# Kernel tuning notes

Measured on AMD Instinct MI355X. Metric: run time of the kernel, lower is better.

## Reference

```python
import jax, jax.numpy as jnp
import numpy as np

T, B, F_, H, D, C = 16, 1024, 512, 128, 8, 100  # trees, batch, feat, hidden, depth, classes
L = 2 ** (D + 1)  # n_leaf = 512


def _routing_tables():
    # Static per-leaf routing: node index and branch side at each depth.
    # Derived from compute_mu's gather indices:
    #   node(d, l) = 2^d - 1 + l // 2^(D+1-d);  side(d, l) = (l // 2^(D-d)) % 2
    l = np.arange(L)
    node = np.stack([(2 ** d - 1) + l // (2 ** (D + 1 - d)) for d in range(D + 1)])  # [D+1, L]
    side = np.stack([(l // (2 ** (D - d))) % 2 for d in range(D + 1)])               # [D+1, L]
    return jnp.asarray(node, dtype=jnp.int32), jnp.asarray(side.astype(np.bool_))


def setup_inputs() -> dict:
    key = jax.random.key(0)
    ks = jax.random.split(key, 4)
    return {
        "feat": jax.random.normal(ks[0], (B, F_), jnp.float32),
        "W1": jax.random.normal(ks[1], (T, F_, H), jnp.float32) * 0.05,
        "b1": jnp.zeros((T, H), jnp.float32),
        "W2": jax.random.normal(ks[2], (T, H, L), jnp.float32) * 0.05,
        "b2": jnp.zeros((T, L), jnp.float32),
        "pi": jax.random.uniform(ks[3], (T, L, C), jnp.float32, -2.0, 2.0),
    }


def reference(feat, W1, b1, W2, b2, pi):
    node, side = _routing_tables()
    # Per-tree MLP head (dropout is identity in eval mode).
    h = jax.nn.relu(jnp.einsum('bf,tfh->tbh', feat, W1) + b1[:, None, :])        # [T,B,H]
    p = jax.nn.sigmoid(jnp.einsum('tbh,thl->tbl', h, W2) + b2[:, None, :])       # [T,B,L]
    # compute_mu: product of routing probs along each root->leaf path.
    sel = p[:, :, node]                          # [T,B,D+1,L] gather (static indices)
    route = jnp.where(side, 1.0 - sel, sel)      # left -> p, right -> 1-p
    mu = jnp.prod(route, axis=2)                 # [T,B,L]
    # compute_py_x: mean over leaves then mean over trees of mu @ softmax(pi).
    leaf_p = jax.nn.softmax(pi, axis=-1)         # [T,L,C]
    py_x = jnp.einsum('tbl,tlc->bc', mu, leaf_p) / (L * T)  # [B,C]
    return jnp.log(py_x)
```

## Files before the change

### kernel.cpp

```cpp
#include <hip/hip_runtime.h>
#include <hip/hip_bf16.h>
#include <math.h>

#define T_ 16
#define B_ 1024
#define F_ 512
#define H_ 128
#define D_ 8
#define C_ 100
#define L_ 512
#define CP_ 112

typedef __attribute__((ext_vector_type(8))) short bf16x8_t;
typedef __attribute__((ext_vector_type(4))) short bf16x4_t;
typedef __attribute__((ext_vector_type(4))) float f32x4_t;

__device__ inline ushort f2bf(float x) {
  __hip_bfloat16 b = __float2bfloat16(x);
  return *(ushort*)&b;
}
__device__ inline float bf2f(ushort u) {
  union { unsigned int i; float f; } v;
  v.i = ((unsigned int)u) << 16;
  return v.f;
}

__global__ __launch_bounds__(256) void k_prep(
    const float* __restrict__ feat, const float* __restrict__ W1,
    const float* __restrict__ W2, const float* __restrict__ pi,
    ushort* __restrict__ feat_bf, ushort* __restrict__ W1T,
    ushort* __restrict__ W2T, ushort* __restrict__ lp) {
  __shared__ float tile[32][33];
  const int bid = blockIdx.x, tid = threadIdx.x;

  if (bid < 256) {
    int i = (bid * 256 + tid) * 8;
    float4 a = *(const float4*)(feat + i);
    float4 b = *(const float4*)(feat + i + 4);
    bf16x8_t o;
    o[0] = (short)f2bf(a.x); o[1] = (short)f2bf(a.y);
    o[2] = (short)f2bf(a.z); o[3] = (short)f2bf(a.w);
    o[4] = (short)f2bf(b.x); o[5] = (short)f2bf(b.y);
    o[6] = (short)f2bf(b.z); o[7] = (short)f2bf(b.w);
    *(bf16x8_t*)(feat_bf + i) = o;
    return;
  }
  if (bid < 2304) {
    const float* X; ushort* XT; int K, N, kb, nb, s;
    if (bid < 1280) {
      int r = bid - 256;  kb = r & 15; nb = (r >> 4) & 3;  s = r >> 6;
      X = W1; XT = W1T; K = F_; N = H_;
    } else {
      int r = bid - 1280; kb = r & 3;  nb = (r >> 2) & 15; s = r >> 6;
      X = W2; XT = W2T; K = H_; N = L_;
    }
    const int k0 = kb * 32, n0 = nb * 32;
    const int c = tid & 31, r0 = tid >> 5;
    const float* Xs = X + (size_t)s * K * N;
    ushort* XTs = XT + (size_t)s * N * K;
#pragma unroll
    for (int j = 0; j < 4; ++j)
      tile[r0 + 8 * j][c] = Xs[(size_t)(k0 + r0 + 8 * j) * N + n0 + c];
    __syncthreads();
#pragma unroll
    for (int j = 0; j < 4; ++j)
      XTs[(size_t)(n0 + r0 + 8 * j) * K + k0 + c] = f2bf(tile[c][r0 + 8 * j]);
    return;
  }
  {
    int row  = (bid - 2304) * 4 + (tid >> 6);
    int lane = tid & 63;
    const float* x = pi + (size_t)row * C_;
    float v0 = (lane < C_) ? x[lane] : -1e30f;
    float v1 = (lane + 64 < C_) ? x[lane + 64] : -1e30f;
    float m = fmaxf(v0, v1);
#pragma unroll
    for (int off = 32; off; off >>= 1) m = fmaxf(m, __shfl_xor(m, off, 64));
    float e0 = __expf(v0 - m);
    float e1 = (lane + 64 < C_) ? __expf(v1 - m) : 0.0f;
    float sm = e0 + e1;
#pragma unroll
    for (int off = 32; off; off >>= 1) sm += __shfl_xor(sm, off, 64);
    float inv = 1.0f / sm;
    size_t base = (size_t)row * CP_;
    if (lane < C_) lp[base + lane] = f2bf(e0 * inv);
    int c2 = lane + 64;
    if (c2 < CP_) lp[base + c2] = f2bf(c2 < C_ ? e1 * inv : 0.0f);
  }
}

__global__ __launch_bounds__(256) void k12_mfma(
    const ushort* __restrict__ feat, const ushort* __restrict__ W1T,
    const float* __restrict__ b1, const ushort* __restrict__ W2T,
    const float* __restrict__ b2, ushort* __restrict__ mu) {
  __shared__ ushort smem[29696];
  ushort (*h_s)[136] = (ushort(*)[136])smem;
  ushort (*a_s)[72]  = (ushort(*)[72])(smem + 4352);
  ushort (*b_s)[72]  = (ushort(*)[72])(smem + 6656);
  ushort (*w_s)[136] = (ushort(*)[136])(smem + 4352);
  ushort (*p_s)[520] = (ushort(*)[520])(smem + 13056);

  const int t = blockIdx.y, b0 = blockIdx.x * 32, tid = threadIdx.x;
  const int w = tid >> 6, lane = tid & 63, quad = lane >> 4, n = lane & 15;

  {
    f32x4_t acc[2][2];
#pragma unroll
    for (int i = 0; i < 2; ++i)
#pragma unroll
      for (int j = 0; j < 2; ++j) acc[i][j] = (f32x4_t){0.f, 0.f, 0.f, 0.f};

    for (int kc = 0; kc < 8; ++kc) {
      __syncthreads();
      {
        int row = tid >> 3, col8 = (tid & 7) * 8;
        *(bf16x8_t*)&a_s[row][col8] =
            *(const bf16x8_t*)(feat + (size_t)(b0 + row) * F_ + kc * 64 + col8);
      }
#pragma unroll
      for (int i = 0; i < 4; ++i) {
        int idx = i * 256 + tid;
        int row = idx >> 3, col8 = (idx & 7) * 8;
        *(bf16x8_t*)&b_s[row][col8] =
            *(const bf16x8_t*)(W1T + ((size_t)t * H_ + row) * F_ + kc * 64 + col8);
      }
      __syncthreads();
#pragma unroll
      for (int ks = 0; ks < 64; ks += 32) {
        bf16x8_t af[2], bfr[2];
#pragma unroll
        for (int mt = 0; mt < 2; ++mt)
          af[mt] = *(const bf16x8_t*)&a_s[mt * 16 + n][ks + quad * 8];
#pragma unroll
        for (int nt = 0; nt < 2; ++nt)
          bfr[nt] = *(const bf16x8_t*)&b_s[w * 32 + nt * 16 + n][ks + quad * 8];
#pragma unroll
        for (int mt = 0; mt < 2; ++mt)
#pragma unroll
          for (int nt = 0; nt < 2; ++nt)
            acc[mt][nt] = __builtin_amdgcn_mfma_f32_16x16x32_bf16(
                af[mt], bfr[nt], acc[mt][nt], 0, 0, 0);
      }
    }
    float bias[2] = {b1[t * H_ + w * 32 + n], b1[t * H_ + w * 32 + 16 + n]};
#pragma unroll
    for (int mt = 0; mt < 2; ++mt)
#pragma unroll
      for (int nt = 0; nt < 2; ++nt)
#pragma unroll
        for (int r = 0; r < 4; ++r) {
          int row = mt * 16 + quad * 4 + r;
          int col = w * 32 + nt * 16 + n;
          float v = acc[mt][nt][r] + bias[nt];
          h_s[row][col] = f2bf(v > 0.f ? v : 0.f);
        }
  }

  for (int nc = 0; nc < 8; ++nc) {
    __syncthreads();
#pragma unroll
    for (int i = 0; i < 4; ++i) {
      int idx = i * 256 + tid;
      int row = idx >> 4, col8 = (idx & 15) * 8;
      *(bf16x8_t*)&w_s[row][col8] =
          *(const bf16x8_t*)(W2T + ((size_t)t * L_ + nc * 64 + row) * H_ + col8);
    }
    __syncthreads();
    f32x4_t acc[2];
    acc[0] = (f32x4_t){0.f, 0.f, 0.f, 0.f};
    acc[1] = (f32x4_t){0.f, 0.f, 0.f, 0.f};
#pragma unroll
    for (int ks = 0; ks < 128; ks += 32) {
      bf16x8_t bfrag = *(const bf16x8_t*)&w_s[w * 16 + n][ks + quad * 8];
#pragma unroll
      for (int mt = 0; mt < 2; ++mt) {
        bf16x8_t afrag = *(const bf16x8_t*)&h_s[mt * 16 + n][ks + quad * 8];
        acc[mt] = __builtin_amdgcn_mfma_f32_16x16x32_bf16(afrag, bfrag,
                                                          acc[mt], 0, 0, 0);
      }
    }
    int l = nc * 64 + w * 16 + n;
    float bias = b2[t * L_ + l];
#pragma unroll
    for (int mt = 0; mt < 2; ++mt)
#pragma unroll
      for (int r = 0; r < 4; ++r) {
        float x = acc[mt][r] + bias;
        p_s[mt * 16 + quad * 4 + r][l] = f2bf(1.0f / (1.0f + __expf(-x)));
      }
  }
  __syncthreads();

#pragma unroll
  for (int pass = 0; pass < 4; ++pass) {
    int b = pass * 8 + (tid >> 5);
    int s = tid & 31;
    float P = 1.f;
#pragma unroll
    for (int d = 0; d < 5; ++d) {
      int nd = (1 << d) - 1 + (s >> (5 - d));
      int sd = (s >> (4 - d)) & 1;
      float pv = bf2f(p_s[b][nd]);
      P *= sd ? (1.f - pv) : pv;
    }
    float p5 = bf2f(p_s[b][31 + s]);
    float q5[2] = {P * p5, P * (1.f - p5)};
    float q6[4], q7[8];
#pragma unroll
    for (int j = 0; j < 2; ++j) {
      float pv = bf2f(p_s[b][63 + 2 * s + j]);
      q6[2 * j] = q5[j] * pv;
      q6[2 * j + 1] = q5[j] * (1.f - pv);
    }
#pragma unroll
    for (int u = 0; u < 4; ++u) {
      float pv = bf2f(p_s[b][127 + 4 * s + u]);
      q7[2 * u] = q6[u] * pv;
      q7[2 * u + 1] = q6[u] * (1.f - pv);
    }
    bf16x8_t o0, o1;
#pragma unroll
    for (int v = 0; v < 8; ++v) {
      float pv = bf2f(p_s[b][255 + 8 * s + v]);
      ushort e0 = f2bf(q7[v] * pv);
      ushort e1 = f2bf(q7[v] * (1.f - pv));
      if (v < 4) { o0[2 * v] = (short)e0; o0[2 * v + 1] = (short)e1; }
      else       { o1[2 * (v - 4)] = (short)e0; o1[2 * (v - 4) + 1] = (short)e1; }
    }
    ushort* dst = mu + ((size_t)t * B_ + b0 + b) * L_ + s * 16;
    *(bf16x8_t*)dst = o0;
    *(bf16x8_t*)(dst + 8) = o1;
  }
}

__global__ __launch_bounds__(256) void k5_mfma(
    const ushort* __restrict__ mu, const ushort* __restrict__ lp,
    float* __restrict__ part) {
  __shared__ ushort bT[CP_ * 68];
  const int t   = blockIdx.y;
  const int m0  = blockIdx.x * 64;
  const int tid = threadIdx.x;
  const int wave = tid >> 6, lane = tid & 63;
  const int quad = lane >> 4;
  const int n    = lane & 15;
  const int mrow = m0 + wave * 16 + n;

  f32x4_t acc[7];
#pragma unroll
  for (int i = 0; i < 7; ++i) acc[i] = (f32x4_t){0.f, 0.f, 0.f, 0.f};

  const ushort* muRow = mu + ((size_t)t * B_ + mrow) * L_;
  const ushort* lp_t  = lp + (size_t)t * L_ * CP_;

  for (int k0 = 0; k0 < L_; k0 += 64) {
    __syncthreads();
#pragma unroll
    for (int i = 0; i < 28; ++i) {
      int e  = i * 256 + tid;
      int kk = e / CP_;
      int c  = e - kk * CP_;
      bT[c * 68 + kk] = lp_t[(size_t)(k0 + kk) * CP_ + c];
    }
    __syncthreads();
#pragma unroll
    for (int ks = 0; ks < 64; ks += 32) {
      bf16x8_t afrag = *(const bf16x8_t*)(muRow + k0 + ks + quad * 8);
#pragma unroll
      for (int nt = 0; nt < 7; ++nt) {
        const ushort* bb = &bT[(nt * 16 + n) * 68 + ks + quad * 8];
        bf16x4_t lo = *(const bf16x4_t*)(bb);
        bf16x4_t hi = *(const bf16x4_t*)(bb + 4);
        bf16x8_t bfrag;
#pragma unroll
        for (int j = 0; j < 4; ++j) { bfrag[j] = lo[j]; bfrag[4 + j] = hi[j]; }
        acc[nt] = __builtin_amdgcn_mfma_f32_16x16x32_bf16(afrag, bfrag, acc[nt], 0, 0, 0);
      }
    }
  }
#pragma unroll
  for (int nt = 0; nt < 7; ++nt) {
    int c = nt * 16 + n;
    if (c < C_) {
#pragma unroll
      for (int r = 0; r < 4; ++r) {
        int m = m0 + wave * 16 + quad * 4 + r;
        part[((size_t)t * B_ + m) * C_ + c] = acc[nt][r];
      }
    }
  }
}

__global__ __launch_bounds__(256) void k6_log(
    const float* __restrict__ part, float* __restrict__ out) {
  int i = blockIdx.x * 256 + threadIdx.x;
  if (i < B_ * C_) {
    float s = 0.0f;
#pragma unroll
    for (int t = 0; t < T_; ++t) s += part[(size_t)t * B_ * C_ + i];
    out[i] = logf(s * (1.0f / (L_ * T_)));
  }
}

extern "C" void kernel_launch(void* const* d_in, const int* in_sizes, int n_in,
                              void* d_out, int out_size, void* d_ws,
                              size_t ws_size, hipStream_t stream) {
  const float* feat = (const float*)d_in[0];
  const float* W1   = (const float*)d_in[1];
  const float* b1   = (const float*)d_in[2];
  const float* W2   = (const float*)d_in[3];
  const float* b2   = (const float*)d_in[4];
  const float* pi   = (const float*)d_in[5];
  float* out = (float*)d_out;

  char* ws = (char*)d_ws;
  ushort* feat_bf  = (ushort*)(ws);
  ushort* W1T_buf  = (ushort*)(ws + ((size_t)1 << 20));
  ushort* W2T_buf  = (ushort*)(ws + ((size_t)3 << 20));
  ushort* mu_buf   = (ushort*)(ws + ((size_t)5 << 20));
  ushort* leaf_buf = (ushort*)(ws + ((size_t)21 << 20));
  float*  part_buf = (float*)(ws + ((size_t)23 << 20));

  k_prep<<<4352, 256, 0, stream>>>(feat, W1, W2, pi, feat_bf, W1T_buf,
                                   W2T_buf, leaf_buf);
  k12_mfma<<<dim3(B_ / 32, T_), 256, 0, stream>>>(feat_bf, W1T_buf, b1,
                                                  W2T_buf, b2, mu_buf);
  k5_mfma<<<dim3(B_ / 64, T_), 256, 0, stream>>>(mu_buf, leaf_buf, part_buf);
  k6_log<<<(B_ * C_ + 255) / 256, 256, 0, stream>>>(part_buf, out);
}
```

Baseline: 114.5 us.

## Fuse leaf-probability GEMM into routing kernel, keep mu in shared memory

The mu @ softmax(pi) GEMM moves into the MLP/routing kernel. The mu tile is written to shared memory over the p_s buffer and consumed directly by MFMA, so the 16 MB bf16 mu array no longer goes to global memory and one kernel launch is removed. The leaf softmax is now stored transposed ([T, C, L]) so B fragments load straight from global memory with no LDS transpose. In exchange, every 32-row block re-reads the per-tree leaf matrix from global/L2, the wave split is uneven (4 vs 3 column tiles), and the prep kernel's transposed writes are strided.

```diff
diff --git a/kernel.cpp b/kernel.cpp
--- a/kernel.cpp
+++ b/kernel.cpp
@@ -29,7 +29,7 @@
     const float* __restrict__ feat, const float* __restrict__ W1,
     const float* __restrict__ W2, const float* __restrict__ pi,
     ushort* __restrict__ feat_bf, ushort* __restrict__ W1T,
-    ushort* __restrict__ W2T, ushort* __restrict__ lp) {
+    ushort* __restrict__ W2T, ushort* __restrict__ lpT) {
   __shared__ float tile[32][33];
   const int bid = blockIdx.x, tid = threadIdx.x;
 
@@ -70,6 +70,7 @@
   {
     int row  = (bid - 2304) * 4 + (tid >> 6);
     int lane = tid & 63;
+    int t = row >> 9, l = row & (L_ - 1);
     const float* x = pi + (size_t)row * C_;
     float v0 = (lane < C_) ? x[lane] : -1e30f;
     float v1 = (lane + 64 < C_) ? x[lane + 64] : -1e30f;
@@ -82,17 +83,18 @@
 #pragma unroll
     for (int off = 32; off; off >>= 1) sm += __shfl_xor(sm, off, 64);
     float inv = 1.0f / sm;
-    size_t base = (size_t)row * CP_;
-    if (lane < C_) lp[base + lane] = f2bf(e0 * inv);
+    ushort* dst = lpT + (size_t)t * CP_ * L_ + l;
+    if (lane < C_) dst[(size_t)lane * L_] = f2bf(e0 * inv);
     int c2 = lane + 64;
-    if (c2 < CP_) lp[base + c2] = f2bf(c2 < C_ ? e1 * inv : 0.0f);
+    if (c2 < CP_) dst[(size_t)c2 * L_] = f2bf(c2 < C_ ? e1 * inv : 0.0f);
   }
 }
 
 __global__ __launch_bounds__(256) void k12_mfma(
     const ushort* __restrict__ feat, const ushort* __restrict__ W1T,
     const float* __restrict__ b1, const ushort* __restrict__ W2T,
-    const float* __restrict__ b2, ushort* __restrict__ mu) {
+    const float* __restrict__ b2, const ushort* __restrict__ lpT,
+    float* __restrict__ part) {
   __shared__ ushort smem[29696];
   ushort (*h_s)[136] = (ushort(*)[136])smem;
   ushort (*a_s)[72]  = (ushort(*)[72])(smem + 4352);
@@ -191,6 +193,7 @@
   }
   __syncthreads();
 
+  bf16x8_t mo[4][2];
 #pragma unroll
   for (int pass = 0; pass < 4; ++pass) {
     int b = pass * 8 + (tid >> 5);
@@ -227,64 +230,49 @@
       if (v < 4) { o0[2 * v] = (short)e0; o0[2 * v + 1] = (short)e1; }
       else       { o1[2 * (v - 4)] = (short)e0; o1[2 * (v - 4) + 1] = (short)e1; }
     }
-    ushort* dst = mu + ((size_t)t * B_ + b0 + b) * L_ + s * 16;
-    *(bf16x8_t*)dst = o0;
-    *(bf16x8_t*)(dst + 8) = o1;
-  }
-}
-
-__global__ __launch_bounds__(256) void k5_mfma(
-    const ushort* __restrict__ mu, const ushort* __restrict__ lp,
-    float* __restrict__ part) {
-  __shared__ ushort bT[CP_ * 68];
-  const int t   = blockIdx.y;
-  const int m0  = blockIdx.x * 64;
-  const int tid = threadIdx.x;
-  const int wave = tid >> 6, lane = tid & 63;
-  const int quad = lane >> 4;
-  const int n    = lane & 15;
-  const int mrow = m0 + wave * 16 + n;
-
-  f32x4_t acc[7];
-#pragma unroll
-  for (int i = 0; i < 7; ++i) acc[i] = (f32x4_t){0.f, 0.f, 0.f, 0.f};
-
-  const ushort* muRow = mu + ((size_t)t * B_ + mrow) * L_;
-  const ushort* lp_t  = lp + (size_t)t * L_ * CP_;
-
-  for (int k0 = 0; k0 < L_; k0 += 64) {
-    __syncthreads();
-#pragma unroll
-    for (int i = 0; i < 28; ++i) {
-      int e  = i * 256 + tid;
-      int kk = e / CP_;
-      int c  = e - kk * CP_;
-      bT[c * 68 + kk] = lp_t[(size_t)(k0 + kk) * CP_ + c];
-    }
-    __syncthreads();
-#pragma unroll
-    for (int ks = 0; ks < 64; ks += 32) {
-      bf16x8_t afrag = *(const bf16x8_t*)(muRow + k0 + ks + quad * 8);
-#pragma unroll
-      for (int nt = 0; nt < 7; ++nt) {
-        const ushort* bb = &bT[(nt * 16 + n) * 68 + ks + quad * 8];
-        bf16x4_t lo = *(const bf16x4_t*)(bb);
-        bf16x4_t hi = *(const bf16x4_t*)(bb + 4);
-        bf16x8_t bfrag;
-#pragma unroll
-        for (int j = 0; j < 4; ++j) { bfrag[j] = lo[j]; bfrag[4 + j] = hi[j]; }
-        acc[nt] = __builtin_amdgcn_mfma_f32_16x16x32_bf16(afrag, bfrag, acc[nt], 0, 0, 0);
-      }
-    }
-  }
-#pragma unroll
-  for (int nt = 0; nt < 7; ++nt) {
-    int c = nt * 16 + n;
-    if (c < C_) {
-#pragma unroll
-      for (int r = 0; r < 4; ++r) {
-        int m = m0 + wave * 16 + quad * 4 + r;
-        part[((size_t)t * B_ + m) * C_ + c] = acc[nt][r];
+    mo[pass][0] = o0;
+    mo[pass][1] = o1;
+  }
+  __syncthreads();
+#pragma unroll
+  for (int pass = 0; pass < 4; ++pass) {
+    int b = pass * 8 + (tid >> 5);
+    int s = tid & 31;
+    *(bf16x8_t*)&p_s[b][s * 16]     = mo[pass][0];
+    *(bf16x8_t*)&p_s[b][s * 16 + 8] = mo[pass][1];
+  }
+  __syncthreads();
+
+  {
+    const int mt = w >> 1;
+    const int nt0 = (w & 1) * 4;
+    const int ncnt = (w & 1) ? 3 : 4;
+    const ushort* arow = &p_s[mt * 16 + n][0];
+    const ushort* brow = lpT + (size_t)t * CP_ * L_ +
+                         ((size_t)(nt0 * 16 + n)) * L_ + quad * 8;
+    f32x4_t acc[4];
+#pragma unroll
+    for (int i = 0; i < 4; ++i) acc[i] = (f32x4_t){0.f, 0.f, 0.f, 0.f};
+#pragma unroll 4
+    for (int k = 0; k < L_; k += 32) {
+      bf16x8_t af = *(const bf16x8_t*)(arow + k + quad * 8);
+#pragma unroll
+      for (int j = 0; j < 4; ++j) {
+        if (j < ncnt) {
+          bf16x8_t bfr = *(const bf16x8_t*)(brow + (size_t)j * 16 * L_ + k);
+          acc[j] = __builtin_amdgcn_mfma_f32_16x16x32_bf16(af, bfr, acc[j],
+                                                           0, 0, 0);
+        }
+      }
+    }
+    const int m0 = b0 + mt * 16 + quad * 4;
+#pragma unroll
+    for (int j = 0; j < 4; ++j) {
+      int c = (nt0 + j) * 16 + n;
+      if (j < ncnt && c < C_) {
+#pragma unroll
+        for (int r = 0; r < 4; ++r)
+          part[((size_t)t * B_ + m0 + r) * C_ + c] = acc[j][r];
       }
     }
   }
@@ -316,14 +304,13 @@
   ushort* feat_bf  = (ushort*)(ws);
   ushort* W1T_buf  = (ushort*)(ws + ((size_t)1 << 20));
   ushort* W2T_buf  = (ushort*)(ws + ((size_t)3 << 20));
-  ushort* mu_buf   = (ushort*)(ws + ((size_t)5 << 20));
-  ushort* leaf_buf = (ushort*)(ws + ((size_t)21 << 20));
-  float*  part_buf = (float*)(ws + ((size_t)23 << 20));
+  ushort* lpT_buf  = (ushort*)(ws + ((size_t)5 << 20));
+  float*  part_buf = (float*)(ws + ((size_t)7 << 20));
 
   k_prep<<<4352, 256, 0, stream>>>(feat, W1, W2, pi, feat_bf, W1T_buf,
-                                   W2T_buf, leaf_buf);
+                                   W2T_buf, lpT_buf);
   k12_mfma<<<dim3(B_ / 32, T_), 256, 0, stream>>>(feat_bf, W1T_buf, b1,
-                                                  W2T_buf, b2, mu_buf);
-  k5_mfma<<<dim3(B_ / 64, T_), 256, 0, stream>>>(mu_buf, leaf_buf, part_buf);
+                                                  W2T_buf, b2, lpT_buf,
+                                                  part_buf);
   k6_log<<<(B_ * C_ + 255) / 256, 256, 0, stream>>>(part_buf, out);
 }
```

Result: no change. 115.8 us (+1.1%).
